# Performance work log

Hardware: AMD Instinct MI355X
Metric: run time of the kernel (lower is better)

## Reference

```python
import jax, jax.numpy as jnp
import numpy as np

N_SRC = 100_000
N_DST = 100_000
N_EDGES = 1_600_000
D_IN = 256
N_HEADS = 4
OUT_FEATS = 32
NEG_SLOPE = 0.2


def setup_inputs() -> dict:
    key = jax.random.key(0)
    k1, k2, k3, k4, k5, k6, k7 = jax.random.split(key, 7)
    return {
        "feat_src": jax.random.normal(k1, (N_SRC, D_IN), dtype=jnp.float32),
        "feat_dst": jax.random.normal(k2, (N_DST, D_IN), dtype=jnp.float32),
        "w_src": jax.random.normal(k3, (D_IN, N_HEADS * OUT_FEATS), dtype=jnp.float32) * 0.05,
        "w_dst": jax.random.normal(k4, (D_IN, N_HEADS * OUT_FEATS), dtype=jnp.float32) * 0.05,
        "attn": jax.random.normal(k5, (N_HEADS, 2 * OUT_FEATS), dtype=jnp.float32) * 0.05,
        "src_idx": jax.random.randint(k6, (N_EDGES,), 0, N_SRC, dtype=jnp.int32),
        "dst_idx": jax.random.randint(k7, (N_EDGES,), 0, N_DST, dtype=jnp.int32),
    }


def reference(feat_src, feat_dst, w_src, w_dst, attn, src_idx, dst_idx):
    H, two_d = attn.shape
    D = two_d // 2
    n_dst = feat_dst.shape[0]
    # node transformations (dropout rate = 0.0 -> identity)
    fs = (feat_src @ w_src).reshape(-1, H, D)   # [Ns, H, D]
    fd = (feat_dst @ w_dst).reshape(-1, H, D)   # [Nd, H, D]
    # per-node attention logits: e_dst uses first half, e_src second half
    e_dst = (fd * attn[:, :D]).sum(-1)          # [Nd, H]
    e_src = (fs * attn[:, D:]).sum(-1)          # [Ns, H]
    # u_add_v on edges + leaky relu
    e = e_src[src_idx] + e_dst[dst_idx]         # [E, H]
    e = jnp.where(e > 0, e, NEG_SLOPE * e)
    # edge softmax: segment softmax over incoming edges of each dst node
    m = jax.ops.segment_max(e, dst_idx, num_segments=n_dst)       # [Nd, H]
    m = jnp.where(jnp.isfinite(m), m, 0.0)                        # empty segments
    ex = jnp.exp(e - m[dst_idx])                                  # [E, H]
    denom = jax.ops.segment_sum(ex, dst_idx, num_segments=n_dst)  # [Nd, H]
    a = ex / denom[dst_idx]                                       # [E, H]
    # u_mul_e + sum aggregation
    msg = fs[src_idx] * a[:, :, None]                             # [E, H, D]
    out = jax.ops.segment_sum(msg, dst_idx, num_segments=n_dst)   # [Nd, H, D]
    return jax.nn.relu(out.reshape(n_dst, H * D))
```

## Files before the change

### kernel.cpp

```cpp
#include <hip/hip_runtime.h>

#define N_NODES 100000
#define N_EDGES 1600000
#define D_IN    256
#define HD      128
#define NEG_SLOPE 0.2f

#define BUK_SH    5
#define BUK_NODES 32
#define NBUCKETS ((N_NODES + BUK_NODES - 1) / BUK_NODES)
#define BUK_CAP  1024
#define BUK_CH   8192
#define NB_BUK   ((N_EDGES + BUK_CH - 1) / BUK_CH)

#define NB_GEMM ((N_NODES + 255) / 256)
#define NB_EDST 1024
#define NB_ZERO ((NBUCKETS + 255) / 256)

#define EX_STRIDE 1032

typedef __bf16 bf16x8 __attribute__((ext_vector_type(8)));
typedef float  f32x4  __attribute__((ext_vector_type(4)));

__device__ __forceinline__ float lrelu_exp(float v) {
  v = v > 0.f ? v : NEG_SLOPE * v;
  return __expf(v);
}
__device__ __forceinline__ float bf_lo(unsigned u) { return __uint_as_float(u << 16); }
__device__ __forceinline__ float bf_hi(unsigned u) { return __uint_as_float(u & 0xffff0000u); }

__global__ __launch_bounds__(256) void prep_kernel(const float* __restrict__ w_src,
                                                   const float* __restrict__ w_dst,
                                                   const float* __restrict__ attn,
                                                   ushort* __restrict__ wT,
                                                   float* __restrict__ v_dst,
                                                   int* __restrict__ bcur) {
  int bid = blockIdx.x;
  int tid = threadIdx.x;
  if (bid < 128) {
    int idx = bid * 256 + tid;
    int k = idx >> 7, n = idx & 127;
    __bf16 bv = (__bf16)w_src[idx];
    wT[n * 256 + k] = *(const ushort*)&bv;
  } else if (bid == 128) {
    int k = tid;
    for (int h = 0; h < 4; ++h) {
      float s = 0.f;
      for (int d = 0; d < 32; ++d)
        s += w_dst[k * HD + h * 32 + d] * attn[h * 64 + d];
      v_dst[k * 4 + h] = s;
    }
  } else {
    int i = (bid - 129) * 256 + tid;
    if (i < NBUCKETS) bcur[i] = 0;
  }
}

__global__ __launch_bounds__(1024) void gemm_kernel(const float* __restrict__ A,
                                                    const ushort* __restrict__ wT16,
                                                    const float* __restrict__ attn,
                                                    unsigned* __restrict__ fs16,
                                                    float* __restrict__ e_src,
                                                    int M) {
  __shared__ ushort Bl[128 * 256];
  const int bid = blockIdx.x;
  const int tid = threadIdx.x;
  const int lane = tid & 63, wid = tid >> 6;
  const int lr = lane & 15, hi = lane >> 4;

  {
    const uint4* wg4 = (const uint4*)wT16;
#pragma unroll
    for (int i = 0; i < 4; ++i) {
      int c = i * 1024 + tid;
      int col = c >> 5;
      unsigned byte = ((unsigned)c * 16u) ^ (((unsigned)col & 31u) << 4);
      *(uint4*)((char*)Bl + byte) = wg4[c];
    }
  }

  f32x4 acc[8];
  const f32x4 zf = {0.f, 0.f, 0.f, 0.f};
#pragma unroll
  for (int n = 0; n < 8; ++n) acc[n] = zf;

  const int bm = bid * 256;
  int row0 = bm + wid * 16 + lr;
  int row0c = row0 < M ? row0 : M - 1;
  const float* a0p = A + (size_t)row0c * D_IN;

  __syncthreads();

#pragma unroll
  for (int ks = 0; ks < 8; ++ks) {
    const int ko = ks * 32 + hi * 8;
    float4 u0 = *(const float4*)(a0p + ko);
    float4 u1 = *(const float4*)(a0p + ko + 4);
    bf16x8 af0;
    af0[0] = (__bf16)u0.x; af0[1] = (__bf16)u0.y; af0[2] = (__bf16)u0.z; af0[3] = (__bf16)u0.w;
    af0[4] = (__bf16)u1.x; af0[5] = (__bf16)u1.y; af0[6] = (__bf16)u1.z; af0[7] = (__bf16)u1.w;
    bf16x8 bf[8];
#pragma unroll
    for (int n = 0; n < 8; ++n) {
      unsigned col = (unsigned)(n * 16 + lr);
      unsigned byte = (col * 512u + (unsigned)(ks * 64 + hi * 16)) ^ ((col & 31u) << 4);
      bf[n] = *(const bf16x8*)((const char*)Bl + byte);
    }
#pragma unroll
    for (int n = 0; n < 8; ++n)
      acc[n] = __builtin_amdgcn_mfma_f32_16x16x32_bf16(af0, bf[n], acc[n], 0, 0, 0);
  }

#pragma unroll
  for (int n = 0; n < 8; ++n) {
#pragma unroll
    for (int r4 = 0; r4 < 4; ++r4) {
      float val = acc[n][r4];
      float pv  = __shfl_xor(val, 1, 64);
      int gr = bm + wid * 16 + hi * 4 + r4;
      if (!(lane & 1) && gr < M) {
        __bf16 b0 = (__bf16)val, b1 = (__bf16)pv;
        unsigned pk = ((unsigned)*(const ushort*)&b1 << 16) | *(const ushort*)&b0;
        fs16[(size_t)gr * 64 + n * 8 + (lr >> 1)] = pk;
      }
    }
  }

#pragma unroll
  for (int gh = 0; gh < 4; ++gh) {
    float av0 = attn[gh * 64 + 32 + lr];
    float av1 = attn[gh * 64 + 48 + lr];
#pragma unroll
    for (int r4 = 0; r4 < 4; ++r4) {
      float s = acc[2 * gh][r4] * av0 + acc[2 * gh + 1][r4] * av1;
      s += __shfl_xor(s, 1, 64);
      s += __shfl_xor(s, 2, 64);
      s += __shfl_xor(s, 4, 64);
      s += __shfl_xor(s, 8, 64);
      int gr = bm + wid * 16 + hi * 4 + r4;
      if (lr == 0 && gr < M) e_src[(size_t)gr * 4 + gh] = s;
    }
  }
}

__global__ __launch_bounds__(256) void edst_kernel(const float* __restrict__ feat_dst,
                                                   const float* __restrict__ v_dst,
                                                   float* __restrict__ e_dst) {
  __shared__ float4 vds[256];
  const int tid = threadIdx.x;
  vds[tid] = ((const float4*)v_dst)[tid];
  __syncthreads();
  const int l = tid & 15;
  const int grp = tid >> 4;
  for (int n = blockIdx.x * 16 + grp; n < N_NODES; n += NB_EDST * 16) {
    const float* fp = feat_dst + (size_t)n * D_IN;
    float ax = 0.f, ay = 0.f, az = 0.f, aw = 0.f;
#pragma unroll
    for (int c = 0; c < 4; ++c) {
      const int k0 = c * 64 + l * 4;
      float4 f = *(const float4*)(fp + k0);
      float4 v0 = vds[k0 + 0], v1 = vds[k0 + 1], v2 = vds[k0 + 2], v3 = vds[k0 + 3];
      ax = fmaf(f.x, v0.x, fmaf(f.y, v1.x, fmaf(f.z, v2.x, fmaf(f.w, v3.x, ax))));
      ay = fmaf(f.x, v0.y, fmaf(f.y, v1.y, fmaf(f.z, v2.y, fmaf(f.w, v3.y, ay))));
      az = fmaf(f.x, v0.z, fmaf(f.y, v1.z, fmaf(f.z, v2.z, fmaf(f.w, v3.z, az))));
      aw = fmaf(f.x, v0.w, fmaf(f.y, v1.w, fmaf(f.z, v2.w, fmaf(f.w, v3.w, aw))));
    }
#pragma unroll
    for (int off = 1; off < 16; off <<= 1) {
      ax += __shfl_xor(ax, off, 64);
      ay += __shfl_xor(ay, off, 64);
      az += __shfl_xor(az, off, 64);
      aw += __shfl_xor(aw, off, 64);
    }
    if (l == 0) *(float4*)(e_dst + (size_t)n * 4) = make_float4(ax, ay, az, aw);
  }
}

__global__ __launch_bounds__(1024) void bucket_kernel(const int* __restrict__ src,
                                                      const int* __restrict__ dstv,
                                                      int* __restrict__ bcur,
                                                      unsigned* __restrict__ ebuk) {
  __shared__ int bh[NBUCKETS];
  const int tid = threadIdx.x;
  const int e0 = blockIdx.x * BUK_CH;
  for (int j = tid; j < NBUCKETS; j += 1024) bh[j] = 0;
  __syncthreads();
  for (int i = tid; i < BUK_CH; i += 1024) {
    int e = e0 + i;
    if (e < N_EDGES) atomicAdd(&bh[dstv[e] >> BUK_SH], 1);
  }
  __syncthreads();
  for (int j = tid; j < NBUCKETS; j += 1024) {
    int c = bh[j];
    bh[j] = (c > 0) ? atomicAdd(&bcur[j], c) : 0;
  }
  __syncthreads();
  for (int i = tid; i < BUK_CH; i += 1024) {
    int e = e0 + i;
    if (e < N_EDGES) {
      int d = dstv[e];
      int b = d >> BUK_SH;
      int p = atomicAdd(&bh[b], 1);
      if (p < BUK_CAP)
        ebuk[(size_t)b * BUK_CAP + p] =
            ((unsigned)src[e] << BUK_SH) | (unsigned)(d & (BUK_NODES - 1));
    }
  }
}

__global__ __launch_bounds__(256) void agg_kernel(const unsigned* __restrict__ ebuk,
                                                  const int* __restrict__ bcur,
                                                  const float4* __restrict__ e_src,
                                                  const float4* __restrict__ e_dst,
                                                  const unsigned* __restrict__ fs16,
                                                  float* __restrict__ out, int N) {
  __shared__ unsigned sorted_e[BUK_CAP];
  __shared__ float ex_s[4][EX_STRIDE];
  __shared__ int lcnt[BUK_NODES];
  __shared__ int lofs_s[BUK_NODES + 1];
  __shared__ int lcur[BUK_NODES];
  const int tid = threadIdx.x;
  const int wslot = tid >> 6;
  const int lane = tid & 63;
  const int lo = blockIdx.x * BUK_NODES;
  const size_t start = (size_t)blockIdx.x * BUK_CAP;
  const int cnt_e = min(bcur[blockIdx.x], BUK_CAP);

  if (tid < BUK_NODES) lcnt[tid] = 0;
  __syncthreads();
  for (int i = tid; i < cnt_e; i += 256)
    atomicAdd(&lcnt[ebuk[start + i] & (BUK_NODES - 1)], 1);
  __syncthreads();
  if (tid == 0) {
    int run = 0;
    for (int j = 0; j < BUK_NODES; ++j) {
      lofs_s[j] = run; lcur[j] = run; run += lcnt[j];
    }
    lofs_s[BUK_NODES] = run;
  }
  __syncthreads();
  for (int i = tid; i < cnt_e; i += 256) {
    unsigned e = ebuk[start + i];
    int p = atomicAdd(&lcur[e & (BUK_NODES - 1)], 1);
    sorted_e[p] = e;
  }
  __syncthreads();

  for (int i = tid; i < cnt_e; i += 256) {
    unsigned ent = sorted_e[i];
    int s  = (int)(ent >> BUK_SH);
    int dl = (int)(ent & (BUK_NODES - 1));
    float4 a  = e_src[s];
    float4 ed = e_dst[lo + dl];
    ex_s[0][i] = lrelu_exp(a.x + ed.x);
    ex_s[1][i] = lrelu_exp(a.y + ed.y);
    ex_s[2][i] = lrelu_exp(a.z + ed.z);
    ex_s[3][i] = lrelu_exp(a.w + ed.w);
  }
  __syncthreads();

  const int g = lane >> 4;
  const int q = lane & 15;
  const int h = q >> 2;

  for (int nl = wslot * 8; nl < wslot * 8 + 8; ++nl) {
    int node = lo + nl;
    if (node >= N) break;
    const int nb = lofs_s[nl], ne = lofs_s[nl + 1];
    float a0=0.f,a1=0.f,a2=0.f,a3=0.f,a4=0.f,a5=0.f,a6=0.f,a7=0.f,den=0.f;

    for (int cb = nb; cb < ne; cb += 16) {
      int e0 = cb + g, e1 = e0 + 4, e2 = e0 + 8, e3 = e0 + 12;
      bool p0 = e0 < ne, p1 = e1 < ne, p2 = e2 < ne, p3 = e3 < ne;
      int c0 = p0 ? e0 : nb, c1 = p1 ? e1 : nb, c2 = p2 ? e2 : nb, c3 = p3 ? e3 : nb;
      int s0 = (int)(sorted_e[c0] >> BUK_SH);
      int s1 = (int)(sorted_e[c1] >> BUK_SH);
      int s2 = (int)(sorted_e[c2] >> BUK_SH);
      int s3 = (int)(sorted_e[c3] >> BUK_SH);
      uint4 u0 = *(const uint4*)(fs16 + (size_t)s0 * 64 + q * 4);
      uint4 u1 = *(const uint4*)(fs16 + (size_t)s1 * 64 + q * 4);
      uint4 u2 = *(const uint4*)(fs16 + (size_t)s2 * 64 + q * 4);
      uint4 u3 = *(const uint4*)(fs16 + (size_t)s3 * 64 + q * 4);
      float x0 = p0 ? ex_s[h][c0] : 0.f;
      float x1 = p1 ? ex_s[h][c1] : 0.f;
      float x2 = p2 ? ex_s[h][c2] : 0.f;
      float x3 = p3 ? ex_s[h][c3] : 0.f;
      a0 = fmaf(x0, bf_lo(u0.x), a0); a1 = fmaf(x0, bf_hi(u0.x), a1);
      a2 = fmaf(x0, bf_lo(u0.y), a2); a3 = fmaf(x0, bf_hi(u0.y), a3);
      a4 = fmaf(x0, bf_lo(u0.z), a4); a5 = fmaf(x0, bf_hi(u0.z), a5);
      a6 = fmaf(x0, bf_lo(u0.w), a6); a7 = fmaf(x0, bf_hi(u0.w), a7);
      a0 = fmaf(x1, bf_lo(u1.x), a0); a1 = fmaf(x1, bf_hi(u1.x), a1);
      a2 = fmaf(x1, bf_lo(u1.y), a2); a3 = fmaf(x1, bf_hi(u1.y), a3);
      a4 = fmaf(x1, bf_lo(u1.z), a4); a5 = fmaf(x1, bf_hi(u1.z), a5);
      a6 = fmaf(x1, bf_lo(u1.w), a6); a7 = fmaf(x1, bf_hi(u1.w), a7);
      a0 = fmaf(x2, bf_lo(u2.x), a0); a1 = fmaf(x2, bf_hi(u2.x), a1);
      a2 = fmaf(x2, bf_lo(u2.y), a2); a3 = fmaf(x2, bf_hi(u2.y), a3);
      a4 = fmaf(x2, bf_lo(u2.z), a4); a5 = fmaf(x2, bf_hi(u2.z), a5);
      a6 = fmaf(x2, bf_lo(u2.w), a6); a7 = fmaf(x2, bf_hi(u2.w), a7);
      a0 = fmaf(x3, bf_lo(u3.x), a0); a1 = fmaf(x3, bf_hi(u3.x), a1);
      a2 = fmaf(x3, bf_lo(u3.y), a2); a3 = fmaf(x3, bf_hi(u3.y), a3);
      a4 = fmaf(x3, bf_lo(u3.z), a4); a5 = fmaf(x3, bf_hi(u3.z), a5);
      a6 = fmaf(x3, bf_lo(u3.w), a6); a7 = fmaf(x3, bf_hi(u3.w), a7);
      den += x0 + x1 + x2 + x3;
    }

    den += __shfl_xor(den, 16, 64); den += __shfl_xor(den, 32, 64);
    a0 += __shfl_xor(a0, 16, 64); a0 += __shfl_xor(a0, 32, 64);
    a1 += __shfl_xor(a1, 16, 64); a1 += __shfl_xor(a1, 32, 64);
    a2 += __shfl_xor(a2, 16, 64); a2 += __shfl_xor(a2, 32, 64);
    a3 += __shfl_xor(a3, 16, 64); a3 += __shfl_xor(a3, 32, 64);
    a4 += __shfl_xor(a4, 16, 64); a4 += __shfl_xor(a4, 32, 64);
    a5 += __shfl_xor(a5, 16, 64); a5 += __shfl_xor(a5, 32, 64);
    a6 += __shfl_xor(a6, 16, 64); a6 += __shfl_xor(a6, 32, 64);
    a7 += __shfl_xor(a7, 16, 64); a7 += __shfl_xor(a7, 32, 64);
    if (lane < 16) {
      float inv = den > 0.f ? 1.f / den : 0.f;
      float4 o1, o2;
      o1.x = fmaxf(a0 * inv, 0.f); o1.y = fmaxf(a1 * inv, 0.f);
      o1.z = fmaxf(a2 * inv, 0.f); o1.w = fmaxf(a3 * inv, 0.f);
      o2.x = fmaxf(a4 * inv, 0.f); o2.y = fmaxf(a5 * inv, 0.f);
      o2.z = fmaxf(a6 * inv, 0.f); o2.w = fmaxf(a7 * inv, 0.f);
      float* op = out + (size_t)node * HD + q * 8;
      *(float4*)(op)     = o1;
      *(float4*)(op + 4) = o2;
    }
  }
}

extern "C" void kernel_launch(void* const* d_in, const int* in_sizes, int n_in,
                              void* d_out, int out_size, void* d_ws, size_t ws_size,
                              hipStream_t stream) {
  const float* feat_src = (const float*)d_in[0];
  const float* feat_dst = (const float*)d_in[1];
  const float* w_src    = (const float*)d_in[2];
  const float* w_dst    = (const float*)d_in[3];
  const float* attn     = (const float*)d_in[4];
  const int*   src_idx  = (const int*)d_in[5];
  const int*   dst_idx  = (const int*)d_in[6];
  float* out = (float*)d_out;
  char* ws = (char*)d_ws;

  unsigned* fs16  = (unsigned*)(ws);
  float*    e_src = (float*)(ws + 25600000);
  float*    e_dst = (float*)(ws + 27200000);
  unsigned* ebuk  = (unsigned*)(ws + 28800000);
  float*    v_dst = (float*)(ws + 41600000);
  ushort*   wT16  = (ushort*)(ws + 41604096);
  int*      bcur  = (int*)  (ws + 41669632);

  prep_kernel<<<129 + NB_ZERO, 256, 0, stream>>>(w_src, w_dst, attn, wT16, v_dst, bcur);

  gemm_kernel<<<NB_GEMM, 1024, 0, stream>>>(feat_src, wT16, attn, fs16, e_src, N_NODES);

  edst_kernel<<<NB_EDST, 256, 0, stream>>>(feat_dst, v_dst, e_dst);

  bucket_kernel<<<NB_BUK, 1024, 0, stream>>>(src_idx, dst_idx, bcur, ebuk);

  agg_kernel<<<NBUCKETS, 256, 0, stream>>>(ebuk, bcur,
      (const float4*)e_src, (const float4*)e_dst, fs16, out, N_NODES);
}
```

Baseline: 170.5 us.

## Merge prep with bucketing and gemm with e_dst into fewer launches

```diff
diff --git a/kernel.cpp b/kernel.cpp
--- a/kernel.cpp
+++ b/kernel.cpp
@@ -14,8 +14,8 @@
 #define NB_BUK   ((N_EDGES + BUK_CH - 1) / BUK_CH)
 
 #define NB_GEMM ((N_NODES + 255) / 256)
-#define NB_EDST 1024
-#define NB_ZERO ((NBUCKETS + 255) / 256)
+#define NB_EDST 256
+#define NB_PREP 33
 
 #define EX_STRIDE 1032
 
@@ -29,181 +29,177 @@
 __device__ __forceinline__ float bf_lo(unsigned u) { return __uint_as_float(u << 16); }
 __device__ __forceinline__ float bf_hi(unsigned u) { return __uint_as_float(u & 0xffff0000u); }
 
-__global__ __launch_bounds__(256) void prep_kernel(const float* __restrict__ w_src,
-                                                   const float* __restrict__ w_dst,
-                                                   const float* __restrict__ attn,
-                                                   ushort* __restrict__ wT,
-                                                   float* __restrict__ v_dst,
-                                                   int* __restrict__ bcur) {
-  int bid = blockIdx.x;
-  int tid = threadIdx.x;
-  if (bid < 128) {
-    int idx = bid * 256 + tid;
+__global__ __launch_bounds__(1024) void prep_bucket_kernel(const float* __restrict__ w_src,
+                                                           const float* __restrict__ w_dst,
+                                                           const float* __restrict__ attn,
+                                                           ushort* __restrict__ wT,
+                                                           float* __restrict__ v_dst,
+                                                           const int* __restrict__ src,
+                                                           const int* __restrict__ dstv,
+                                                           int* __restrict__ bcur,
+                                                           unsigned* __restrict__ ebuk) {
+  const int bid = blockIdx.x;
+  const int tid = threadIdx.x;
+  if (bid < 32) {
+    int idx = bid * 1024 + tid;
     int k = idx >> 7, n = idx & 127;
     __bf16 bv = (__bf16)w_src[idx];
     wT[n * 256 + k] = *(const ushort*)&bv;
-  } else if (bid == 128) {
-    int k = tid;
-    for (int h = 0; h < 4; ++h) {
-      float s = 0.f;
-      for (int d = 0; d < 32; ++d)
-        s += w_dst[k * HD + h * 32 + d] * attn[h * 64 + d];
-      v_dst[k * 4 + h] = s;
+  } else if (bid == 32) {
+    if (tid < 256) {
+      int k = tid;
+      for (int h = 0; h < 4; ++h) {
+        float s = 0.f;
+        for (int d = 0; d < 32; ++d)
+          s += w_dst[k * HD + h * 32 + d] * attn[h * 64 + d];
+        v_dst[k * 4 + h] = s;
+      }
     }
   } else {
-    int i = (bid - 129) * 256 + tid;
-    if (i < NBUCKETS) bcur[i] = 0;
-  }
-}
-
-__global__ __launch_bounds__(1024) void gemm_kernel(const float* __restrict__ A,
-                                                    const ushort* __restrict__ wT16,
-                                                    const float* __restrict__ attn,
-                                                    unsigned* __restrict__ fs16,
-                                                    float* __restrict__ e_src,
-                                                    int M) {
+    __shared__ int bh[NBUCKETS];
+    const int e0 = (bid - NB_PREP) * BUK_CH;
+    for (int j = tid; j < NBUCKETS; j += 1024) bh[j] = 0;
+    __syncthreads();
+    for (int i = tid; i < BUK_CH; i += 1024) {
+      int e = e0 + i;
+      if (e < N_EDGES) atomicAdd(&bh[dstv[e] >> BUK_SH], 1);
+    }
+    __syncthreads();
+    for (int j = tid; j < NBUCKETS; j += 1024) {
+      int c = bh[j];
+      bh[j] = (c > 0) ? atomicAdd(&bcur[j], c) : 0;
+    }
+    __syncthreads();
+    for (int i = tid; i < BUK_CH; i += 1024) {
+      int e = e0 + i;
+      if (e < N_EDGES) {
+        int d = dstv[e];
+        int b = d >> BUK_SH;
+        int p = atomicAdd(&bh[b], 1);
+        if (p < BUK_CAP)
+          ebuk[(size_t)b * BUK_CAP + p] =
+              ((unsigned)src[e] << BUK_SH) | (unsigned)(d & (BUK_NODES - 1));
+      }
+    }
+  }
+}
+
+__global__ __launch_bounds__(1024) void gemm_edst_kernel(const float* __restrict__ A,
+                                                         const ushort* __restrict__ wT16,
+                                                         const float* __restrict__ attn,
+                                                         unsigned* __restrict__ fs16,
+                                                         float* __restrict__ e_src,
+                                                         const float* __restrict__ feat_dst,
+                                                         const float* __restrict__ v_dst,
+                                                         float* __restrict__ e_dst,
+                                                         int M) {
   __shared__ ushort Bl[128 * 256];
   const int bid = blockIdx.x;
   const int tid = threadIdx.x;
   const int lane = tid & 63, wid = tid >> 6;
   const int lr = lane & 15, hi = lane >> 4;
 
-  {
-    const uint4* wg4 = (const uint4*)wT16;
-#pragma unroll
-    for (int i = 0; i < 4; ++i) {
-      int c = i * 1024 + tid;
-      int col = c >> 5;
-      unsigned byte = ((unsigned)c * 16u) ^ (((unsigned)col & 31u) << 4);
-      *(uint4*)((char*)Bl + byte) = wg4[c];
-    }
-  }
-
-  f32x4 acc[8];
-  const f32x4 zf = {0.f, 0.f, 0.f, 0.f};
-#pragma unroll
-  for (int n = 0; n < 8; ++n) acc[n] = zf;
-
-  const int bm = bid * 256;
-  int row0 = bm + wid * 16 + lr;
-  int row0c = row0 < M ? row0 : M - 1;
-  const float* a0p = A + (size_t)row0c * D_IN;
-
-  __syncthreads();
-
-#pragma unroll
-  for (int ks = 0; ks < 8; ++ks) {
-    const int ko = ks * 32 + hi * 8;
-    float4 u0 = *(const float4*)(a0p + ko);
-    float4 u1 = *(const float4*)(a0p + ko + 4);
-    bf16x8 af0;
-    af0[0] = (__bf16)u0.x; af0[1] = (__bf16)u0.y; af0[2] = (__bf16)u0.z; af0[3] = (__bf16)u0.w;
-    af0[4] = (__bf16)u1.x; af0[5] = (__bf16)u1.y; af0[6] = (__bf16)u1.z; af0[7] = (__bf16)u1.w;
-    bf16x8 bf[8];
+  if (bid < NB_GEMM) {
+    {
+      const uint4* wg4 = (const uint4*)wT16;
+#pragma unroll
+      for (int i = 0; i < 4; ++i) {
+        int c = i * 1024 + tid;
+        int col = c >> 5;
+        unsigned byte = ((unsigned)c * 16u) ^ (((unsigned)col & 31u) << 4);
+        *(uint4*)((char*)Bl + byte) = wg4[c];
+      }
+    }
+
+    f32x4 acc[8];
+    const f32x4 zf = {0.f, 0.f, 0.f, 0.f};
+#pragma unroll
+    for (int n = 0; n < 8; ++n) acc[n] = zf;
+
+    const int bm = bid * 256;
+    int row0 = bm + wid * 16 + lr;
+    int row0c = row0 < M ? row0 : M - 1;
+    const float* a0p = A + (size_t)row0c * D_IN;
+
+    __syncthreads();
+
+#pragma unroll
+    for (int ks = 0; ks < 8; ++ks) {
+      const int ko = ks * 32 + hi * 8;
+      float4 u0 = *(const float4*)(a0p + ko);
+      float4 u1 = *(const float4*)(a0p + ko + 4);
+      bf16x8 af0;
+      af0[0] = (__bf16)u0.x; af0[1] = (__bf16)u0.y; af0[2] = (__bf16)u0.z; af0[3] = (__bf16)u0.w;
+      af0[4] = (__bf16)u1.x; af0[5] = (__bf16)u1.y; af0[6] = (__bf16)u1.z; af0[7] = (__bf16)u1.w;
+      bf16x8 bf[8];
+#pragma unroll
+      for (int n = 0; n < 8; ++n) {
+        unsigned col = (unsigned)(n * 16 + lr);
+        unsigned byte = (col * 512u + (unsigned)(ks * 64 + hi * 16)) ^ ((col & 31u) << 4);
+        bf[n] = *(const bf16x8*)((const char*)Bl + byte);
+      }
+#pragma unroll
+      for (int n = 0; n < 8; ++n)
+        acc[n] = __builtin_amdgcn_mfma_f32_16x16x32_bf16(af0, bf[n], acc[n], 0, 0, 0);
+    }
+
 #pragma unroll
     for (int n = 0; n < 8; ++n) {
-      unsigned col = (unsigned)(n * 16 + lr);
-      unsigned byte = (col * 512u + (unsigned)(ks * 64 + hi * 16)) ^ ((col & 31u) << 4);
-      bf[n] = *(const bf16x8*)((const char*)Bl + byte);
-    }
-#pragma unroll
-    for (int n = 0; n < 8; ++n)
-      acc[n] = __builtin_amdgcn_mfma_f32_16x16x32_bf16(af0, bf[n], acc[n], 0, 0, 0);
-  }
-
-#pragma unroll
-  for (int n = 0; n < 8; ++n) {
-#pragma unroll
-    for (int r4 = 0; r4 < 4; ++r4) {
-      float val = acc[n][r4];
-      float pv  = __shfl_xor(val, 1, 64);
-      int gr = bm + wid * 16 + hi * 4 + r4;
-      if (!(lane & 1) && gr < M) {
-        __bf16 b0 = (__bf16)val, b1 = (__bf16)pv;
-        unsigned pk = ((unsigned)*(const ushort*)&b1 << 16) | *(const ushort*)&b0;
-        fs16[(size_t)gr * 64 + n * 8 + (lr >> 1)] = pk;
-      }
-    }
-  }
-
-#pragma unroll
-  for (int gh = 0; gh < 4; ++gh) {
-    float av0 = attn[gh * 64 + 32 + lr];
-    float av1 = attn[gh * 64 + 48 + lr];
-#pragma unroll
-    for (int r4 = 0; r4 < 4; ++r4) {
-      float s = acc[2 * gh][r4] * av0 + acc[2 * gh + 1][r4] * av1;
-      s += __shfl_xor(s, 1, 64);
-      s += __shfl_xor(s, 2, 64);
-      s += __shfl_xor(s, 4, 64);
-      s += __shfl_xor(s, 8, 64);
-      int gr = bm + wid * 16 + hi * 4 + r4;
-      if (lr == 0 && gr < M) e_src[(size_t)gr * 4 + gh] = s;
-    }
-  }
-}
-
-__global__ __launch_bounds__(256) void edst_kernel(const float* __restrict__ feat_dst,
-                                                   const float* __restrict__ v_dst,
-                                                   float* __restrict__ e_dst) {
-  __shared__ float4 vds[256];
-  const int tid = threadIdx.x;
-  vds[tid] = ((const float4*)v_dst)[tid];
-  __syncthreads();
-  const int l = tid & 15;
-  const int grp = tid >> 4;
-  for (int n = blockIdx.x * 16 + grp; n < N_NODES; n += NB_EDST * 16) {
-    const float* fp = feat_dst + (size_t)n * D_IN;
-    float ax = 0.f, ay = 0.f, az = 0.f, aw = 0.f;
-#pragma unroll
-    for (int c = 0; c < 4; ++c) {
-      const int k0 = c * 64 + l * 4;
-      float4 f = *(const float4*)(fp + k0);
-      float4 v0 = vds[k0 + 0], v1 = vds[k0 + 1], v2 = vds[k0 + 2], v3 = vds[k0 + 3];
-      ax = fmaf(f.x, v0.x, fmaf(f.y, v1.x, fmaf(f.z, v2.x, fmaf(f.w, v3.x, ax))));
-      ay = fmaf(f.x, v0.y, fmaf(f.y, v1.y, fmaf(f.z, v2.y, fmaf(f.w, v3.y, ay))));
-      az = fmaf(f.x, v0.z, fmaf(f.y, v1.z, fmaf(f.z, v2.z, fmaf(f.w, v3.z, az))));
-      aw = fmaf(f.x, v0.w, fmaf(f.y, v1.w, fmaf(f.z, v2.w, fmaf(f.w, v3.w, aw))));
-    }
-#pragma unroll
-    for (int off = 1; off < 16; off <<= 1) {
-      ax += __shfl_xor(ax, off, 64);
-      ay += __shfl_xor(ay, off, 64);
-      az += __shfl_xor(az, off, 64);
-      aw += __shfl_xor(aw, off, 64);
-    }
-    if (l == 0) *(float4*)(e_dst + (size_t)n * 4) = make_float4(ax, ay, az, aw);
-  }
-}
-
-__global__ __launch_bounds__(1024) void bucket_kernel(const int* __restrict__ src,
-                                                      const int* __restrict__ dstv,
-                                                      int* __restrict__ bcur,
-                                                      unsigned* __restrict__ ebuk) {
-  __shared__ int bh[NBUCKETS];
-  const int tid = threadIdx.x;
-  const int e0 = blockIdx.x * BUK_CH;
-  for (int j = tid; j < NBUCKETS; j += 1024) bh[j] = 0;
-  __syncthreads();
-  for (int i = tid; i < BUK_CH; i += 1024) {
-    int e = e0 + i;
-    if (e < N_EDGES) atomicAdd(&bh[dstv[e] >> BUK_SH], 1);
-  }
-  __syncthreads();
-  for (int j = tid; j < NBUCKETS; j += 1024) {
-    int c = bh[j];
-    bh[j] = (c > 0) ? atomicAdd(&bcur[j], c) : 0;
-  }
-  __syncthreads();
-  for (int i = tid; i < BUK_CH; i += 1024) {
-    int e = e0 + i;
-    if (e < N_EDGES) {
-      int d = dstv[e];
-      int b = d >> BUK_SH;
-      int p = atomicAdd(&bh[b], 1);
-      if (p < BUK_CAP)
-        ebuk[(size_t)b * BUK_CAP + p] =
-            ((unsigned)src[e] << BUK_SH) | (unsigned)(d & (BUK_NODES - 1));
+#pragma unroll
+      for (int r4 = 0; r4 < 4; ++r4) {
+        float val = acc[n][r4];
+        float pv  = __shfl_xor(val, 1, 64);
+        int gr = bm + wid * 16 + hi * 4 + r4;
+        if (!(lane & 1) && gr < M) {
+          __bf16 b0 = (__bf16)val, b1 = (__bf16)pv;
+          unsigned pk = ((unsigned)*(const ushort*)&b1 << 16) | *(const ushort*)&b0;
+          fs16[(size_t)gr * 64 + n * 8 + (lr >> 1)] = pk;
+        }
+      }
+    }
+
+#pragma unroll
+    for (int gh = 0; gh < 4; ++gh) {
+      float av0 = attn[gh * 64 + 32 + lr];
+      float av1 = attn[gh * 64 + 48 + lr];
+#pragma unroll
+      for (int r4 = 0; r4 < 4; ++r4) {
+        float s = acc[2 * gh][r4] * av0 + acc[2 * gh + 1][r4] * av1;
+        s += __shfl_xor(s, 1, 64);
+        s += __shfl_xor(s, 2, 64);
+        s += __shfl_xor(s, 4, 64);
+        s += __shfl_xor(s, 8, 64);
+        int gr = bm + wid * 16 + hi * 4 + r4;
+        if (lr == 0 && gr < M) e_src[(size_t)gr * 4 + gh] = s;
+      }
+    }
+  } else {
+    float4* vds = (float4*)Bl;
+    if (tid < 256) vds[tid] = ((const float4*)v_dst)[tid];
+    __syncthreads();
+    const int l = tid & 15;
+    const int grp = tid >> 4;
+    for (int n = (bid - NB_GEMM) * 64 + grp; n < N_NODES; n += NB_EDST * 64) {
+      const float* fp = feat_dst + (size_t)n * D_IN;
+      float ax = 0.f, ay = 0.f, az = 0.f, aw = 0.f;
+#pragma unroll
+      for (int c = 0; c < 4; ++c) {
+        const int k0 = c * 64 + l * 4;
+        float4 f = *(const float4*)(fp + k0);
+        float4 v0 = vds[k0 + 0], v1 = vds[k0 + 1], v2 = vds[k0 + 2], v3 = vds[k0 + 3];
+        ax = fmaf(f.x, v0.x, fmaf(f.y, v1.x, fmaf(f.z, v2.x, fmaf(f.w, v3.x, ax))));
+        ay = fmaf(f.x, v0.y, fmaf(f.y, v1.y, fmaf(f.z, v2.y, fmaf(f.w, v3.y, ay))));
+        az = fmaf(f.x, v0.z, fmaf(f.y, v1.z, fmaf(f.z, v2.z, fmaf(f.w, v3.z, az))));
+        aw = fmaf(f.x, v0.w, fmaf(f.y, v1.w, fmaf(f.z, v2.w, fmaf(f.w, v3.w, aw))));
+      }
+#pragma unroll
+      for (int off = 1; off < 16; off <<= 1) {
+        ax += __shfl_xor(ax, off, 64);
+        ay += __shfl_xor(ay, off, 64);
+        az += __shfl_xor(az, off, 64);
+        aw += __shfl_xor(aw, off, 64);
+      }
+      if (l == 0) *(float4*)(e_dst + (size_t)n * 4) = make_float4(ax, ay, az, aw);
     }
   }
 }
@@ -348,13 +344,13 @@
   ushort*   wT16  = (ushort*)(ws + 41604096);
   int*      bcur  = (int*)  (ws + 41669632);
 
-  prep_kernel<<<129 + NB_ZERO, 256, 0, stream>>>(w_src, w_dst, attn, wT16, v_dst, bcur);
-
-  gemm_kernel<<<NB_GEMM, 1024, 0, stream>>>(feat_src, wT16, attn, fs16, e_src, N_NODES);
-
-  edst_kernel<<<NB_EDST, 256, 0, stream>>>(feat_dst, v_dst, e_dst);
-
-  bucket_kernel<<<NB_BUK, 1024, 0, stream>>>(src_idx, dst_idx, bcur, ebuk);
+  hipMemsetAsync(bcur, 0, NBUCKETS * sizeof(int), stream);
+
+  prep_bucket_kernel<<<NB_PREP + NB_BUK, 1024, 0, stream>>>(
+      w_src, w_dst, attn, wT16, v_dst, src_idx, dst_idx, bcur, ebuk);
+
+  gemm_edst_kernel<<<NB_GEMM + NB_EDST, 1024, 0, stream>>>(
+      feat_src, wT16, attn, fs16, e_src, feat_dst, v_dst, e_dst, N_NODES);
 
   agg_kernel<<<NBUCKETS, 256, 0, stream>>>(ebuk, bcur,
       (const float4*)e_src, (const float4*)e_dst, fs16, out, N_NODES);
```

New measurement: 164.9 us, median of 2. 3.3% less time.
